# Optimization experiments

Measured on AMD Instinct MI355X. Metric: run time of the kernel, lower is better.

The kernel has to match this reference:

```python
import jax, jax.numpy as jnp
import numpy as np

TOP_K = 4

def _silu_and_mul(gu):
    g, u = jnp.split(gu, 2, axis=-1)
    return jax.nn.silu(g) * u

def setup_inputs() -> dict:
    key = jax.random.key(0)
    ks = jax.random.split(key, 7)
    H, E, I, Is = 2048, 16, 1408, 5632
    s = 0.02
    return {
        "hidden_states": jax.random.normal(ks[0], (4, 1024, H), dtype=jnp.float32),
        "gate_w": jax.random.normal(ks[1], (E, H), dtype=jnp.float32) * s,
        "sgate_w": jax.random.normal(ks[2], (1, H), dtype=jnp.float32) * s,
        "w13": jax.random.normal(ks[3], (E, 2 * I, H), dtype=jnp.float32) * s,
        "w2": jax.random.normal(ks[4], (E, H, I), dtype=jnp.float32) * s,
        "shared_gate_up_w": jax.random.normal(ks[5], (2 * Is, H), dtype=jnp.float32) * s,
        "shared_down_w": jax.random.normal(ks[6], (H, Is), dtype=jnp.float32) * s,
    }

def reference(hidden_states, gate_w, sgate_w, w13, w2, shared_gate_up_w, shared_down_w):
    B, S, H = hidden_states.shape
    x = hidden_states.reshape(-1, H)  # [M, H]
    E = gate_w.shape[0]

    # shared expert: SiluAndMul MLP gated by sigmoid(shared_expert_gate(x))
    shared = _silu_and_mul(x @ shared_gate_up_w.T) @ shared_down_w.T
    shared = shared * jax.nn.sigmoid(x @ sgate_w.T)  # [M, H]

    # router: softmax in fp32, top-k (NOT renormalized, per original code)
    router_logits = x @ gate_w.T
    routing_weights = jax.nn.softmax(router_logits.astype(jnp.float32), axis=-1)
    topk_w, topk_ids = jax.lax.top_k(routing_weights, TOP_K)  # [M, K]

    # loop over fixed expert set via scan; every token goes through each
    # expert, masked by its routing coefficient (0 if not routed)
    def body(acc, ew):
        w13_e, w2_e, e = ew
        coef = jnp.sum(jnp.where(topk_ids == e, topk_w, 0.0), axis=-1)  # [M]
        h = _silu_and_mul(x @ w13_e.T)  # [M, I]
        acc = acc + (h @ w2_e.T).astype(jnp.float32) * coef[:, None]
        return acc, None

    init = jnp.zeros((x.shape[0], H), dtype=jnp.float32)
    sparse_out, _ = jax.lax.scan(body, init, (w13, w2, jnp.arange(E)))
    out = shared + sparse_out.astype(x.dtype)
    return out.reshape(B, S, H)
```

## Files before the change

kernel.cpp:

```cpp
#include <hip/hip_runtime.h>
#include <hip/hip_bf16.h>

#define E_NUM 16
#define TOPK 4
#define H_DIM 2048
#define I_DIM 1408
#define IS_DIM 5632
#define M_TOK 4096

typedef __attribute__((ext_vector_type(8))) short short8;
typedef __attribute__((ext_vector_type(4))) float f32x4;

static __device__ __forceinline__ unsigned short f2bf(float f) {
    unsigned int u = __float_as_uint(f);
    unsigned int r = (u + 0x7FFFu + ((u >> 16) & 1u)) >> 16;
    return (unsigned short)r;
}

static __device__ __forceinline__ void gl16(const unsigned short* g, unsigned short* l) {
    __builtin_amdgcn_global_load_lds(
        (const __attribute__((address_space(1))) unsigned int*)g,
        (__attribute__((address_space(3))) unsigned int*)l, 16, 0, 0);
}

__global__ __launch_bounds__(256) void k_router(
    const float* __restrict__ x, const float* __restrict__ gw,
    const float* __restrict__ sgw, int* __restrict__ counts,
    int* __restrict__ ltok, float* __restrict__ lcoef, float* __restrict__ sg)
{
    const int wid = threadIdx.x >> 6, lane = threadIdx.x & 63;
    const int t = blockIdx.x * 4 + wid;
    const float* xr = x + (size_t)t * H_DIM;
    float xv[32];
#pragma unroll
    for (int i = 0; i < 32; ++i) xv[i] = xr[i * 64 + lane];

    float lg[E_NUM];
    for (int e = 0; e < E_NUM; ++e) {
        const float* g = gw + (size_t)e * H_DIM;
        float s = 0.f;
#pragma unroll
        for (int i = 0; i < 32; ++i) s += xv[i] * g[i * 64 + lane];
#pragma unroll
        for (int off = 32; off; off >>= 1) s += __shfl_xor(s, off);
        lg[e] = s;
    }
    {
        float s = 0.f;
#pragma unroll
        for (int i = 0; i < 32; ++i) s += xv[i] * sgw[i * 64 + lane];
#pragma unroll
        for (int off = 32; off; off >>= 1) s += __shfl_xor(s, off);
        if (lane == 0) sg[t] = 1.f / (1.f + __expf(-s));
    }
    float mx = lg[0];
#pragma unroll
    for (int e = 1; e < E_NUM; ++e) mx = fmaxf(mx, lg[e]);
    float sum = 0.f, w[E_NUM];
#pragma unroll
    for (int e = 0; e < E_NUM; ++e) { w[e] = __expf(lg[e] - mx); sum += w[e]; }
    float inv = 1.f / sum;
#pragma unroll
    for (int e = 0; e < E_NUM; ++e) w[e] *= inv;

    if (lane == 0) {
        for (int j = 0; j < TOPK; ++j) {
            float best = -1.f; int bi = 0;
            for (int e = 0; e < E_NUM; ++e) if (w[e] > best) { best = w[e]; bi = e; }
            int pos = atomicAdd(&counts[bi], 1);
            ltok[bi * M_TOK + pos]  = t;
            lcoef[bi * M_TOK + pos] = best;
            w[bi] = -2.f;
        }
    }
}

__global__ void k_prefix(const int* __restrict__ counts, int* __restrict__ base) {
    if (threadIdx.x == 0) {
        int a = 0;
        for (int e = 0; e < E_NUM; ++e) { base[e] = a; a += counts[e]; }
        base[E_NUM] = a;
    }
}

__global__ __launch_bounds__(256) void k_cvtall(
    const float* __restrict__ x, const float* __restrict__ sguw,
    const float* __restrict__ sdw, const float* __restrict__ w13,
    const float* __restrict__ w2,
    unsigned short* __restrict__ xb, unsigned short* __restrict__ sguwb,
    unsigned short* __restrict__ sdwb, unsigned short* __restrict__ w13b,
    unsigned short* __restrict__ w2b)
{
    const size_t N0 = 1048576;
    const size_t N1 = 3932160;
    const size_t N2 = 5373952;
    const size_t N3 = 16908288;
    const size_t N4 = 22675456;
    size_t stride = (size_t)gridDim.x * 256;
    for (size_t t = (size_t)blockIdx.x * 256 + threadIdx.x; t < N4; t += stride) {
        const float* s; unsigned short* d;
        if (t < N0) {
            size_t i = t * 8; s = x + i; d = xb + i;
        } else if (t < N1) {
            size_t i = (t - N0) * 8;
            unsigned drow = (unsigned)(i >> 11), col = (unsigned)(i & 2047u);
            unsigned q = drow >> 4, rm = drow & 15u;
            unsigned srow = ((q >> 1) << 4) + rm + ((q & 1u) ? (unsigned)IS_DIM : 0u);
            s = sguw + ((size_t)srow << 11) + col; d = sguwb + i;
        } else if (t < N2) {
            size_t i = (t - N1) * 8; s = sdw + i; d = sdwb + i;
        } else if (t < N3) {
            size_t i = (t - N2) * 8;
            unsigned drow = (unsigned)(i >> 11), col = (unsigned)(i & 2047u);
            unsigned grp = drow / (2 * I_DIM), rr = drow - grp * (2 * I_DIM);
            unsigned q = rr >> 4, rm = rr & 15u;
            unsigned srow = ((q >> 1) << 4) + rm + ((q & 1u) ? (unsigned)I_DIM : 0u);
            s = w13 + (((size_t)grp * (2 * I_DIM) + srow) << 11) + col; d = w13b + i;
        } else {
            size_t i = (t - N3) * 8; s = w2 + i; d = w2b + i;
        }
        float4 a = *(const float4*)s;
        float4 b = *(const float4*)(s + 4);
        union { unsigned short u[8]; short8 v; } o;
        o.u[0] = f2bf(a.x); o.u[1] = f2bf(a.y); o.u[2] = f2bf(a.z); o.u[3] = f2bf(a.w);
        o.u[4] = f2bf(b.x); o.u[5] = f2bf(b.y); o.u[6] = f2bf(b.z); o.u[7] = f2bf(b.w);
        *(short8*)d = o.v;
    }
}

template<int MODE, int KDIM, int KCH, long long BSTR>
__device__ __forceinline__ void gemm_body(
    const unsigned short* __restrict__ Abase,
    const unsigned short* __restrict__ Bbase,
    void* __restrict__ outp,
    const int* __restrict__ ltok, const float* __restrict__ lcoef,
    const int* __restrict__ counts, const int* __restrict__ basearr,
    const float* __restrict__ sg,
    unsigned short* smem, const int n0, const int r0, const int e, const int kbeg)
{
    constexpr bool UP = (MODE == 0 || MODE == 2);
    constexpr int OSTR = (MODE == 0) ? IS_DIM : I_DIM;
    constexpr int NT = KCH / 64;

    unsigned short* sA = smem;
    unsigned short* sB = smem + 49152;

    const int tid = threadIdx.x;
    const int lane = tid & 63, wid = tid >> 6;
    const int wr = wid >> 1, wc = wid & 1;
    const int lr = lane & 15, lk = lane >> 4;

    int cnt = M_TOK, gbase = 0;
    if constexpr (MODE == 2 || MODE == 3) {
        cnt = counts[e];
        if (r0 >= cnt) return;
        gbase = basearr[e];
    }
    const unsigned short* Bexp = Bbase + (size_t)e * (size_t)BSTR;

    const unsigned short* aptr[2][2];
#pragma unroll
    for (int h = 0; h < 2; ++h) {
#pragma unroll
        for (int i = 0; i < 2; ++i) {
            const int eo = (i * 512 + tid) * 8;
            const int prow = eo >> 6;
            const int kch = ((eo >> 3) & 7) ^ (prow & 7);
            const int lrow = h * 128 + prow;
            int ar;
            if constexpr (MODE == 0 || MODE == 1) ar = r0 + lrow;
            else {
                int rr2 = r0 + lrow; if (rr2 > cnt - 1) rr2 = cnt - 1;
                ar = (MODE == 2) ? ltok[e * M_TOK + rr2] : (gbase + rr2);
            }
            aptr[h][i] = Abase + (size_t)ar * KDIM + kbeg + kch * 8;
        }
    }
    const unsigned short* bptr[2];
#pragma unroll
    for (int i = 0; i < 2; ++i) {
        const int eo = (i * 512 + tid) * 8;
        const int prow = eo >> 6;
        const int kch = ((eo >> 3) & 7) ^ (prow & 7);
        bptr[i] = Bexp + (size_t)(n0 + prow) * KDIM + kbeg + kch * 8;
    }

    f32x4 acc[4][4];
    const f32x4 z = {0.f, 0.f, 0.f, 0.f};
#pragma unroll
    for (int m = 0; m < 4; ++m)
#pragma unroll
        for (int n = 0; n < 4; ++n) acc[m][n] = z;

    auto STAGE = [&](int buf, int kt) {
#pragma unroll
        for (int i = 0; i < 2; ++i)
            gl16(aptr[0][i] + kt, &sA[buf * 16384 + (i * 512 + tid) * 8]);
#pragma unroll
        for (int i = 0; i < 2; ++i)
            gl16(aptr[1][i] + kt, &sA[buf * 16384 + 8192 + (i * 512 + tid) * 8]);
#pragma unroll
        for (int i = 0; i < 2; ++i)
            gl16(bptr[i] + kt, &sB[buf * 8192 + (i * 512 + tid) * 8]);
    };

    STAGE(0, 0);
    STAGE(1, 64);
    asm volatile("s_waitcnt vmcnt(6)" ::: "memory");
    __builtin_amdgcn_s_barrier();

    short8 af[8], bf[8];
    int rb = 0;

#pragma unroll 1
    for (int t = 0; t < NT; ++t) {
        const bool pf = (t + 2 < NT);
        int wb = rb + 2; if (wb >= 3) wb -= 3;
        const int cbA = rb * 16384, cbB = rb * 8192;

#pragma unroll
        for (int m = 0; m < 4; ++m) {
            const int row = wr * 64 + m * 16 + lr;
#pragma unroll
            for (int kk = 0; kk < 2; ++kk)
                af[m * 2 + kk] = *(const short8*)&sA[cbA + (row << 6) + ((((kk << 2) + lk) ^ (row & 7)) << 3)];
        }
#pragma unroll
        for (int n = 0; n < 4; ++n) {
            const int row = wc * 64 + n * 16 + lr;
#pragma unroll
            for (int kk = 0; kk < 2; ++kk)
                bf[n * 2 + kk] = *(const short8*)&sB[cbB + (row << 6) + ((((kk << 2) + lk) ^ (row & 7)) << 3)];
        }

        if (pf) STAGE(wb, (t + 2) * 64);

        __builtin_amdgcn_s_setprio(1);
#pragma unroll
        for (int kk = 0; kk < 2; ++kk)
#pragma unroll
            for (int n = 0; n < 4; ++n)
#pragma unroll
                for (int m = 0; m < 4; ++m)
                    acc[m][n] = __builtin_amdgcn_mfma_f32_16x16x32_bf16(af[m * 2 + kk], bf[n * 2 + kk], acc[m][n], 0, 0, 0);
        __builtin_amdgcn_s_setprio(0);

        if (pf) asm volatile("s_waitcnt vmcnt(6)" ::: "memory");
        else    asm volatile("s_waitcnt vmcnt(0)" ::: "memory");
        __builtin_amdgcn_s_barrier();

        rb = (rb + 1 == 3) ? 0 : rb + 1;
    }

    if constexpr (UP) {
        const int hc0 = (n0 >> 1) + wc * 32 + lr;
        unsigned short* hb = (unsigned short*)outp;
#pragma unroll
        for (int m = 0; m < 4; ++m) {
#pragma unroll
            for (int j = 0; j < 4; ++j) {
                const int r = wr * 64 + m * 16 + lk * 4 + j;
                bool ok; size_t orow;
                if constexpr (MODE == 0) { ok = true; orow = (size_t)(r0 + r) * OSTR; }
                else { ok = (r0 + r < cnt); orow = (size_t)(gbase + r0 + r) * OSTR; }
                if (ok) {
                    float g0 = acc[m][0][j], u0 = acc[m][1][j];
                    float g1 = acc[m][2][j], u1 = acc[m][3][j];
                    hb[orow + hc0]      = f2bf(g0 / (1.f + __expf(-g0)) * u0);
                    hb[orow + hc0 + 16] = f2bf(g1 / (1.f + __expf(-g1)) * u1);
                }
            }
        }
    } else {
        float* op = (float*)outp;
#pragma unroll
        for (int m = 0; m < 4; ++m) {
#pragma unroll
            for (int j = 0; j < 4; ++j) {
                const int r = wr * 64 + m * 16 + lk * 4 + j;
                int tok; float scale; bool ok;
                if constexpr (MODE == 1) {
                    tok = r0 + r; scale = sg[tok]; ok = true;
                } else {
                    ok = (r0 + r < cnt);
                    int idx = ok ? (e * M_TOK + r0 + r) : (e * M_TOK);
                    tok = ltok[idx]; scale = lcoef[idx];
                }
                if (ok) {
                    size_t orow = (size_t)tok * H_DIM;
#pragma unroll
                    for (int n = 0; n < 4; ++n) {
                        const int col = n0 + wc * 64 + n * 16 + lr;
                        atomicAdd(op + orow + col, acc[m][n][j] * scale);
                    }
                }
            }
        }
    }
}

static __device__ __forceinline__ void xcd_swz(int& n0, int& r0) {
    const unsigned gx = gridDim.x, gy = gridDim.y;
    const unsigned nwg = gx * gy;
    const unsigned orig = blockIdx.y * gx + blockIdx.x;
    const unsigned q8 = nwg >> 3, r8 = nwg & 7;
    const unsigned xcd = orig & 7, off8 = orig >> 3;
    const unsigned wg = ((xcd < r8) ? xcd * (q8 + 1) : r8 * (q8 + 1) + (xcd - r8) * q8) + off8;
    n0 = (int)(wg / gy) * 128;
    r0 = (int)(wg % gy) * 256;
}

template<int MODE, int KDIM, int KCH, long long BSTR>
__global__ __launch_bounds__(512, 2) void k_gemm(
    const unsigned short* __restrict__ Abase,
    const unsigned short* __restrict__ Bbase,
    void* __restrict__ outp,
    const int* __restrict__ ltok, const float* __restrict__ lcoef,
    const int* __restrict__ counts, const int* __restrict__ basearr,
    const float* __restrict__ sg)
{
    extern __shared__ unsigned short smem[];
    int n0, r0;
    xcd_swz(n0, r0);
    gemm_body<MODE, KDIM, KCH, BSTR>(Abase, Bbase, outp, ltok, lcoef, counts,
                                     basearr, sg, smem, n0, r0, blockIdx.z, 0);
}

__global__ __launch_bounds__(512, 2) void k_down(
    const unsigned short* __restrict__ hs,
    const unsigned short* __restrict__ he,
    const unsigned short* __restrict__ sdwb,
    const unsigned short* __restrict__ w2b,
    float* __restrict__ out,
    const int* __restrict__ ltok, const float* __restrict__ lcoef,
    const int* __restrict__ counts, const int* __restrict__ basearr,
    const float* __restrict__ sg)
{
    extern __shared__ unsigned short smem[];
    int n0, r0;
    xcd_swz(n0, r0);
    const int z = blockIdx.z;
    if (z < 2) {
        gemm_body<1, 5632, 2816, 0LL>(hs, sdwb, out, ltok, lcoef, counts,
                                      basearr, sg, smem, n0, r0, 0, z * 2816);
    } else {
        gemm_body<3, 1408, 1408, 2883584LL>(he, w2b, out, ltok, lcoef, counts,
                                            basearr, sg, smem, n0, r0, z - 2, 0);
    }
}

extern "C" void kernel_launch(void* const* d_in, const int* in_sizes, int n_in,
                              void* d_out, int out_size, void* d_ws, size_t ws_size,
                              hipStream_t stream) {
    const float* x    = (const float*)d_in[0];
    const float* gw   = (const float*)d_in[1];
    const float* sgw  = (const float*)d_in[2];
    const float* w13  = (const float*)d_in[3];
    const float* w2   = (const float*)d_in[4];
    const float* sguw = (const float*)d_in[5];
    const float* sdw  = (const float*)d_in[6];
    float* out = (float*)d_out;

    char* ws = (char*)d_ws;
    unsigned short* xb    = (unsigned short*)ws;
    unsigned short* hbuf  = (unsigned short*)(ws + 16777216);
    unsigned short* w13b  = (unsigned short*)(ws + 62914560);
    unsigned short* w2b   = (unsigned short*)(ws + 247463936);
    unsigned short* sguwb = (unsigned short*)(ws + 339738624);
    unsigned short* sdwb  = (unsigned short*)(ws + 385875968);
    unsigned short* he    = sguwb;
    size_t so = 408944640ULL;
    int*   ltok   = (int*)  (ws + so);
    float* lcoef  = (float*)(ws + so + 262144);
    int*   counts = (int*)  (ws + so + 524288);
    int*   basep  = (int*)  (ws + so + 524288 + 256);
    float* sg     = (float*)(ws + so + 524288 + 512);

    hipMemsetAsync(counts, 0, 64, stream);
    hipMemsetAsync(out, 0, (size_t)out_size * sizeof(float), stream);
    k_router<<<M_TOK / 4, 256, 0, stream>>>(x, gw, sgw, counts, ltok, lcoef, sg);
    k_prefix<<<1, 64, 0, stream>>>(counts, basep);
    k_cvtall<<<8192, 256, 0, stream>>>(x, sguw, sdw, w13, w2,
                                       xb, sguwb, sdwb, w13b, w2b);

    static const int DYN = 147456;
    (void)hipFuncSetAttribute(reinterpret_cast<const void*>(&k_gemm<0, 2048, 2048, 0LL>),
                              hipFuncAttributeMaxDynamicSharedMemorySize, DYN);
    (void)hipFuncSetAttribute(reinterpret_cast<const void*>(&k_gemm<2, 2048, 2048, 5767168LL>),
                              hipFuncAttributeMaxDynamicSharedMemorySize, DYN);
    (void)hipFuncSetAttribute(reinterpret_cast<const void*>(&k_down),
                              hipFuncAttributeMaxDynamicSharedMemorySize, DYN);

    k_gemm<0, 2048, 2048, 0LL>
        <<<dim3(2 * IS_DIM / 128, M_TOK / 256, 1), 512, DYN, stream>>>(
            xb, sguwb, hbuf, ltok, lcoef, counts, basep, sg);
    k_gemm<2, 2048, 2048, 5767168LL>
        <<<dim3(2 * I_DIM / 128, M_TOK / 256, E_NUM), 512, DYN, stream>>>(
            xb, w13b, he, ltok, lcoef, counts, basep, sg);
    k_down<<<dim3(H_DIM / 128, M_TOK / 256, 2 + E_NUM), 512, DYN, stream>>>(
        hbuf, he, sdwb, w2b, out, ltok, lcoef, counts, basep, sg);
}
```

Measured before the change: 1.196 ms.

## Split down-projection into direct-store shared GEMM followed by atomic expert GEMM

The combined down kernel, which split the shared-expert K across two blocks and used atomics for everything, is replaced by two launches. The shared-expert down GEMM now runs over the full K in one block and stores its result directly. That removes both the output memset and the atomics on the shared path. The routed-expert GEMM then accumulates into the output with atomics, which costs an extra launch, serialises the two GEMMs, and halves the shared-path parallelism (256 blocks, each doing the full K).

```diff
diff --git a/kernel.cpp b/kernel.cpp
--- a/kernel.cpp
+++ b/kernel.cpp
@@ -139,6 +139,7 @@
     unsigned short* smem, const int n0, const int r0, const int e, const int kbeg)
 {
     constexpr bool UP = (MODE == 0 || MODE == 2);
+    constexpr bool DIRECT = (MODE == 1 && KCH == KDIM);
     constexpr int OSTR = (MODE == 0) ? IS_DIM : I_DIM;
     constexpr int NT = KCH / 64;
 
@@ -291,7 +292,10 @@
 #pragma unroll
                     for (int n = 0; n < 4; ++n) {
                         const int col = n0 + wc * 64 + n * 16 + lr;
-                        atomicAdd(op + orow + col, acc[m][n][j] * scale);
+                        if constexpr (DIRECT)
+                            op[orow + col] = acc[m][n][j] * scale;
+                        else
+                            atomicAdd(op + orow + col, acc[m][n][j] * scale);
                     }
                 }
             }
@@ -326,29 +330,6 @@
                                      basearr, sg, smem, n0, r0, blockIdx.z, 0);
 }
 
-__global__ __launch_bounds__(512, 2) void k_down(
-    const unsigned short* __restrict__ hs,
-    const unsigned short* __restrict__ he,
-    const unsigned short* __restrict__ sdwb,
-    const unsigned short* __restrict__ w2b,
-    float* __restrict__ out,
-    const int* __restrict__ ltok, const float* __restrict__ lcoef,
-    const int* __restrict__ counts, const int* __restrict__ basearr,
-    const float* __restrict__ sg)
-{
-    extern __shared__ unsigned short smem[];
-    int n0, r0;
-    xcd_swz(n0, r0);
-    const int z = blockIdx.z;
-    if (z < 2) {
-        gemm_body<1, 5632, 2816, 0LL>(hs, sdwb, out, ltok, lcoef, counts,
-                                      basearr, sg, smem, n0, r0, 0, z * 2816);
-    } else {
-        gemm_body<3, 1408, 1408, 2883584LL>(he, w2b, out, ltok, lcoef, counts,
-                                            basearr, sg, smem, n0, r0, z - 2, 0);
-    }
-}
-
 extern "C" void kernel_launch(void* const* d_in, const int* in_sizes, int n_in,
                               void* d_out, int out_size, void* d_ws, size_t ws_size,
                               hipStream_t stream) {
@@ -377,7 +358,6 @@
     float* sg     = (float*)(ws + so + 524288 + 512);
 
     hipMemsetAsync(counts, 0, 64, stream);
-    hipMemsetAsync(out, 0, (size_t)out_size * sizeof(float), stream);
     k_router<<<M_TOK / 4, 256, 0, stream>>>(x, gw, sgw, counts, ltok, lcoef, sg);
     k_prefix<<<1, 64, 0, stream>>>(counts, basep);
     k_cvtall<<<8192, 256, 0, stream>>>(x, sguw, sdw, w13, w2,
@@ -388,7 +368,9 @@
                               hipFuncAttributeMaxDynamicSharedMemorySize, DYN);
     (void)hipFuncSetAttribute(reinterpret_cast<const void*>(&k_gemm<2, 2048, 2048, 5767168LL>),
                               hipFuncAttributeMaxDynamicSharedMemorySize, DYN);
-    (void)hipFuncSetAttribute(reinterpret_cast<const void*>(&k_down),
+    (void)hipFuncSetAttribute(reinterpret_cast<const void*>(&k_gemm<1, 5632, 5632, 0LL>),
+                              hipFuncAttributeMaxDynamicSharedMemorySize, DYN);
+    (void)hipFuncSetAttribute(reinterpret_cast<const void*>(&k_gemm<3, 1408, 1408, 2883584LL>),
                               hipFuncAttributeMaxDynamicSharedMemorySize, DYN);
 
     k_gemm<0, 2048, 2048, 0LL>
@@ -397,6 +379,10 @@
     k_gemm<2, 2048, 2048, 5767168LL>
         <<<dim3(2 * I_DIM / 128, M_TOK / 256, E_NUM), 512, DYN, stream>>>(
             xb, w13b, he, ltok, lcoef, counts, basep, sg);
-    k_down<<<dim3(H_DIM / 128, M_TOK / 256, 2 + E_NUM), 512, DYN, stream>>>(
-        hbuf, he, sdwb, w2b, out, ltok, lcoef, counts, basep, sg);
-}
+    k_gemm<1, 5632, 5632, 0LL>
+        <<<dim3(H_DIM / 128, M_TOK / 256, 1), 512, DYN, stream>>>(
+            hbuf, sdwb, out, ltok, lcoef, counts, basep, sg);
+    k_gemm<3, 1408, 1408, 2883584LL>
+        <<<dim3(H_DIM / 128, M_TOK / 256, E_NUM), 512, DYN, stream>>>(
+            he, w2b, out, ltok, lcoef, counts, basep, sg);
+}
```

Measured after the change: 1.147 ms. 4.1% less time.
